# Kernel optimization log

Hardware: AMD Instinct MI355X
Metric: run time of the kernel (lower is better)

Reference implementation:

```python
import jax, jax.numpy as jnp
import numpy as np
import math

B, NB, HID, KD, NH = 256, 16, 512, 64, 8

def setup_inputs() -> dict:
    key = jax.random.key(0)
    ks = jax.random.split(key, 6)
    s = lambda fan_in: 1.0 / math.sqrt(fan_in)
    return {
        "h": jax.random.normal(ks[0], (B, NB, HID), dtype=jnp.float32),
        "mask": jax.random.randint(ks[1], (B, NB), 0, 2, dtype=jnp.int32),
        "Wk": jax.random.normal(ks[2], (NB, HID, KD * NH), dtype=jnp.float32) * s(HID),
        "Wq": jax.random.normal(ks[3], (NB, HID, KD * NH), dtype=jnp.float32) * s(HID),
        "Wv": jax.random.normal(ks[4], (NB, HID, HID * NH), dtype=jnp.float32) * s(HID),
        "Wo": jax.random.normal(ks[5], (NB, HID * NH, HID), dtype=jnp.float32) * s(HID * NH),
    }

def _group_linear(x, w):
    # x: (B, NB, din), w: (NB, din, dout) -> (B, NB, dout)
    return jnp.einsum('bnd,nde->bne', x, w)

def reference(h, mask, Wk, Wq, Wv, Wo):
    # grouped QKV projections
    k = _group_linear(h, Wk).reshape(B, NB, NH, KD).transpose(0, 2, 1, 3)    # (B,H,NB,KD)
    q = _group_linear(h, Wq).reshape(B, NB, NH, KD).transpose(0, 2, 1, 3)    # (B,H,NB,KD)
    v = _group_linear(h, Wv).reshape(B, NB, NH, HID).transpose(0, 2, 1, 3)   # (B,H,NB,HID)
    scores = jnp.einsum('bhqd,bhkd->bhqk', q, k) / math.sqrt(KD)             # (B,H,NB,NB)
    probs = jax.nn.softmax(scores, axis=-1)
    # post-softmax row mask: mask (B,NB) -> (B,1,NB,1)
    probs = probs * mask.astype(probs.dtype)[:, None, :, None]
    ctx = jnp.einsum('bhqk,bhkd->bhqd', probs, v)                            # (B,H,NB,HID)
    ctx = ctx.transpose(0, 2, 1, 3).reshape(B, NB, NH * HID)                 # (B,NB,H*HID)
    return _group_linear(ctx, Wo)                                            # (B,NB,HID)
```

## Files before the change

kernel.cpp:

```cpp
#include <hip/hip_runtime.h>


typedef short s16x4 __attribute__((ext_vector_type(4)));
typedef short s16x8 __attribute__((ext_vector_type(8)));
typedef float f32x4 __attribute__((ext_vector_type(4)));

__device__ __forceinline__ unsigned short f2bf(float f) {
  unsigned int u = __builtin_bit_cast(unsigned int, f);
  u += 0x7fffu + ((u >> 16) & 1u);
  return (unsigned short)(u >> 16);
}
__device__ __forceinline__ float bf2f(unsigned short s) {
  unsigned int u = ((unsigned int)s) << 16;
  return __builtin_bit_cast(float, u);
}

__global__ __launch_bounds__(256) void cvt_h(const float* __restrict__ h,
                                             unsigned short* __restrict__ hb)
{
  int i = (blockIdx.x * 256 + threadIdx.x) * 4;
  float4 v = *reinterpret_cast<const float4*>(h + i);
  s16x4 st = { (short)f2bf(v.x), (short)f2bf(v.y), (short)f2bf(v.z), (short)f2bf(v.w) };
  *reinterpret_cast<s16x4*>(hb + i) = st;
}

__global__ __launch_bounds__(256) void qkv_gemm(
    const unsigned short* __restrict__ hb, const float* __restrict__ Wq,
    const float* __restrict__ Wk, const float* __restrict__ Wv,
    unsigned short* __restrict__ qo, unsigned short* __restrict__ ko,
    unsigned short* __restrict__ vo)
{
  const int g    = blockIdx.y;
  const int n0   = blockIdx.x * 64;
  const int tid  = threadIdx.x;
  const int lane = tid & 63;
  const int wave = tid >> 6;
  const int wm   = wave * 64;

  const float* W; unsigned short* out; size_t obase; int oldc, wN, c0;
  if (n0 < 512)       { W = Wq + (size_t)g * 262144;  out = qo; obase = (size_t)g * 512;  oldc = 8192;  wN = 512;  c0 = n0; }
  else if (n0 < 1024) { W = Wk + (size_t)g * 262144;  out = ko; obase = (size_t)g * 512;  oldc = 8192;  wN = 512;  c0 = n0 - 512; }
  else                { W = Wv + (size_t)g * 2097152; out = vo; obase = (size_t)g * 4096; oldc = 65536; wN = 4096; c0 = n0 - 1024; }

  const unsigned short* A = hb + (size_t)g * 512;

  __shared__ unsigned short As[256][32];
  __shared__ unsigned short Bs[64][36];

  f32x4 acc[4][4];
  #pragma unroll
  for (int i = 0; i < 4; i++)
    #pragma unroll
    for (int j = 0; j < 4; j++) acc[i][j] = (f32x4){0.f, 0.f, 0.f, 0.f};

  const int fr = lane & 15, fq = lane >> 4;

  for (int k0 = 0; k0 < 512; k0 += 32) {
    __syncthreads();
    #pragma unroll
    for (int p = 0; p < 4; p++) {
      int idx = p * 256 + tid;
      int row = idx >> 2, kq = idx & 3;
      *reinterpret_cast<s16x8*>(&As[row][kq * 8]) =
          *reinterpret_cast<const s16x8*>(A + (size_t)row * 8192 + k0 + kq * 8);
    }
    #pragma unroll
    for (int p = 0; p < 2; p++) {
      int idx = p * 256 + tid;
      int n = idx & 63, kc = idx >> 6;
      const float* wp = W + (size_t)(k0 + kc * 4) * wN + c0 + n;
      float w0 = wp[0], w1 = wp[wN], w2 = wp[2 * wN], w3 = wp[3 * wN];
      s16x4 st = { (short)f2bf(w0), (short)f2bf(w1), (short)f2bf(w2), (short)f2bf(w3) };
      *reinterpret_cast<s16x4*>(&Bs[n][kc * 4]) = st;
    }
    __syncthreads();
    s16x8 af[4], bfr[4];
    #pragma unroll
    for (int mi = 0; mi < 4; mi++)
      af[mi] = *reinterpret_cast<const s16x8*>(&As[wm + mi * 16 + fr][fq * 8]);
    #pragma unroll
    for (int ni = 0; ni < 4; ni++) {
      const s16x4* bp = reinterpret_cast<const s16x4*>(&Bs[ni * 16 + fr][fq * 8]);
      s16x4 lo = bp[0], hi = bp[1];
      bfr[ni] = __builtin_shufflevector(lo, hi, 0, 1, 2, 3, 4, 5, 6, 7);
    }
    #pragma unroll
    for (int mi = 0; mi < 4; mi++)
      #pragma unroll
      for (int ni = 0; ni < 4; ni++)
        acc[mi][ni] = __builtin_amdgcn_mfma_f32_16x16x32_bf16(af[mi], bfr[ni], acc[mi][ni], 0, 0, 0);
  }

  #pragma unroll
  for (int mi = 0; mi < 4; mi++)
    #pragma unroll
    for (int ni = 0; ni < 4; ni++)
      #pragma unroll
      for (int r = 0; r < 4; r++) {
        int row = wm + mi * 16 + fq * 4 + r;
        int col = c0 + ni * 16 + fr;
        out[obase + (size_t)row * oldc + col] = f2bf(acc[mi][ni][r]);
      }
}

__global__ __launch_bounds__(256) void attn_kernel(
    const unsigned short* __restrict__ q, const unsigned short* __restrict__ k,
    const unsigned short* __restrict__ v, const int* __restrict__ mask,
    unsigned short* __restrict__ ctx)
{
  const int b  = blockIdx.x >> 3;
  const int hh = blockIdx.x & 7;
  const int tid = threadIdx.x;

  __shared__ float qs[16][65];
  __shared__ float ks[16][65];
  __shared__ float sc[16][16];

  {
    int n = tid >> 4, d4 = (tid & 15) * 4;
    size_t gi = ((size_t)(b * 16 + n) << 9) + (hh << 6) + d4;
    ushort4 qv = *reinterpret_cast<const ushort4*>(q + gi);
    ushort4 kv = *reinterpret_cast<const ushort4*>(k + gi);
    qs[n][d4] = bf2f(qv.x); qs[n][d4+1] = bf2f(qv.y); qs[n][d4+2] = bf2f(qv.z); qs[n][d4+3] = bf2f(qv.w);
    ks[n][d4] = bf2f(kv.x); ks[n][d4+1] = bf2f(kv.y); ks[n][d4+2] = bf2f(kv.z); ks[n][d4+3] = bf2f(kv.w);
  }
  __syncthreads();
  {
    int qi = tid >> 4, ki = tid & 15;
    float s = 0.f;
    #pragma unroll
    for (int j = 0; j < 64; j++) s += qs[qi][j] * ks[ki][j];
    sc[qi][ki] = s * 0.125f;
  }
  __syncthreads();
  if (tid < 16) {
    float m = sc[tid][0];
    #pragma unroll
    for (int j = 1; j < 16; j++) m = fmaxf(m, sc[tid][j]);
    float ev[16], sum = 0.f;
    #pragma unroll
    for (int j = 0; j < 16; j++) { ev[j] = __expf(sc[tid][j] - m); sum += ev[j]; }
    float scale = (mask[b * 16 + tid] != 0) ? (1.f / sum) : 0.f;
    #pragma unroll
    for (int j = 0; j < 16; j++) sc[tid][j] = ev[j] * scale;
  }
  __syncthreads();
  {
    int col4  = (tid & 127) * 4;
    int qbase = (tid >> 7) * 8;
    float a0[8], a1[8], a2[8], a3[8];
    #pragma unroll
    for (int j = 0; j < 8; j++) { a0[j] = 0.f; a1[j] = 0.f; a2[j] = 0.f; a3[j] = 0.f; }
    #pragma unroll
    for (int kk = 0; kk < 16; kk++) {
      ushort4 vv = *reinterpret_cast<const ushort4*>(
          v + ((size_t)(b * 16 + kk) << 12) + (hh << 9) + col4);
      float v0 = bf2f(vv.x), v1 = bf2f(vv.y), v2 = bf2f(vv.z), v3 = bf2f(vv.w);
      #pragma unroll
      for (int j = 0; j < 8; j++) {
        float p = sc[qbase + j][kk];
        a0[j] += p * v0; a1[j] += p * v1; a2[j] += p * v2; a3[j] += p * v3;
      }
    }
    #pragma unroll
    for (int j = 0; j < 8; j++) {
      ushort4 st = { f2bf(a0[j]), f2bf(a1[j]), f2bf(a2[j]), f2bf(a3[j]) };
      *reinterpret_cast<ushort4*>(
          ctx + ((size_t)(b * 16 + qbase + j) << 12) + (hh << 9) + col4) = st;
    }
  }
}

__global__ __launch_bounds__(512) void out_gemm(
    const unsigned short* __restrict__ ctxp, const float* __restrict__ Wo,
    float* __restrict__ partial)
{
  const int g    = blockIdx.y;
  const int bx   = blockIdx.x;
  const int sk   = bx >> 3;
  const int n0   = (bx & 7) * 64;
  const int tid  = threadIdx.x;
  const int lane = tid & 63;
  const int wave = tid >> 6;
  const int wm   = (wave >> 1) * 64;
  const int wn   = (wave & 1) * 32;

  const unsigned short* A = ctxp + (size_t)g * 4096;
  const float* W = Wo + (size_t)g * 2097152;

  __shared__ unsigned short As[256][32];
  __shared__ unsigned short Bs[64][36];

  f32x4 acc[4][2];
  #pragma unroll
  for (int i = 0; i < 4; i++)
    #pragma unroll
    for (int j = 0; j < 2; j++) acc[i][j] = (f32x4){0.f, 0.f, 0.f, 0.f};

  const int fr = lane & 15, fq = lane >> 4;
  const int kend = sk * 1024 + 1024;

  for (int k0 = sk * 1024; k0 < kend; k0 += 32) {
    __syncthreads();
    #pragma unroll
    for (int p = 0; p < 2; p++) {
      int idx = p * 512 + tid;
      int row = idx >> 2, kq = idx & 3;
      *reinterpret_cast<s16x8*>(&As[row][kq * 8]) =
          *reinterpret_cast<const s16x8*>(A + (size_t)row * 65536 + k0 + kq * 8);
    }
    {
      int n = tid & 63, kc = tid >> 6;
      const float* wp = W + (size_t)(k0 + kc * 4) * 512 + n0 + n;
      float w0 = wp[0], w1 = wp[512], w2 = wp[1024], w3 = wp[1536];
      s16x4 st = { (short)f2bf(w0), (short)f2bf(w1), (short)f2bf(w2), (short)f2bf(w3) };
      *reinterpret_cast<s16x4*>(&Bs[n][kc * 4]) = st;
    }
    __syncthreads();
    s16x8 af[4], bfr[2];
    #pragma unroll
    for (int mi = 0; mi < 4; mi++)
      af[mi] = *reinterpret_cast<const s16x8*>(&As[wm + mi * 16 + fr][fq * 8]);
    #pragma unroll
    for (int ni = 0; ni < 2; ni++) {
      const s16x4* bp = reinterpret_cast<const s16x4*>(&Bs[wn + ni * 16 + fr][fq * 8]);
      s16x4 lo = bp[0], hi = bp[1];
      bfr[ni] = __builtin_shufflevector(lo, hi, 0, 1, 2, 3, 4, 5, 6, 7);
    }
    #pragma unroll
    for (int mi = 0; mi < 4; mi++)
      #pragma unroll
      for (int ni = 0; ni < 2; ni++)
        acc[mi][ni] = __builtin_amdgcn_mfma_f32_16x16x32_bf16(af[mi], bfr[ni], acc[mi][ni], 0, 0, 0);
  }

  float* pg = partial + (size_t)sk * 2097152 + (size_t)g * 512;
  #pragma unroll
  for (int mi = 0; mi < 4; mi++)
    #pragma unroll
    for (int ni = 0; ni < 2; ni++)
      #pragma unroll
      for (int r = 0; r < 4; r++) {
        int row = wm + mi * 16 + fq * 4 + r;
        int col = n0 + wn + ni * 16 + fr;
        pg[(size_t)row * 8192 + col] = acc[mi][ni][r];
      }
}

__global__ __launch_bounds__(256) void reduce4(const float* __restrict__ part,
                                               float* __restrict__ out)
{
  int i = (blockIdx.x * 256 + threadIdx.x) * 4;
  float4 a = *reinterpret_cast<const float4*>(part + i);
  float4 b = *reinterpret_cast<const float4*>(part + 2097152 + i);
  float4 c = *reinterpret_cast<const float4*>(part + 4194304 + i);
  float4 d = *reinterpret_cast<const float4*>(part + 6291456 + i);
  float4 s = { a.x + b.x + c.x + d.x, a.y + b.y + c.y + d.y,
               a.z + b.z + c.z + d.z, a.w + b.w + c.w + d.w };
  *reinterpret_cast<float4*>(out + i) = s;
}

extern "C" void kernel_launch(void* const* d_in, const int* in_sizes, int n_in,
                              void* d_out, int out_size, void* d_ws, size_t ws_size,
                              hipStream_t stream) {
  const float* h  = (const float*)d_in[0];
  const int* mask = (const int*)d_in[1];
  const float* Wk = (const float*)d_in[2];
  const float* Wq = (const float*)d_in[3];
  const float* Wv = (const float*)d_in[4];
  const float* Wo = (const float*)d_in[5];
  float* out = (float*)d_out;

  unsigned short* qws   = (unsigned short*)d_ws;
  unsigned short* kws   = qws + 2097152;
  unsigned short* vws   = kws + 2097152;
  unsigned short* ctxws = vws + 16777216;
  unsigned short* hb    = ctxws;
  float* part           = (float*)d_ws;

  cvt_h<<<2048, 256, 0, stream>>>(h, hb);
  qkv_gemm<<<dim3(80, 16), 256, 0, stream>>>(hb, Wq, Wk, Wv, qws, kws, vws);
  attn_kernel<<<2048, 256, 0, stream>>>(qws, kws, vws, mask, ctxws);
  out_gemm<<<dim3(32, 16), 512, 0, stream>>>(ctxws, Wo, part);
  reduce4<<<2048, 256, 0, stream>>>(part, out);
}
```

Before: 388.0 us.

## Retile QKV and output GEMMs to 128x128 with register prefetch and atomic split-K

Both grouped GEMMs now use 128x128 output tiles with 64-deep K steps and 8 waves per block. The next K tile is prefetched into registers with vectorized float4 weight loads while MFMAs run on the current shared-memory tile. The output GEMM splits K eight ways and accumulates into a zeroed output with atomicAdd, which removes the partial-sum buffer and the separate reduce kernel. In exchange it adds atomic contention, a memset and nondeterministic summation order, and the larger tiles may lower occupancy.

```diff
diff --git a/kernel.cpp b/kernel.cpp
--- a/kernel.cpp
+++ b/kernel.cpp
@@ -24,81 +24,105 @@
   *reinterpret_cast<s16x4*>(hb + i) = st;
 }
 
-__global__ __launch_bounds__(256) void qkv_gemm(
+__global__ __launch_bounds__(512) void qkv_gemm(
     const unsigned short* __restrict__ hb, const float* __restrict__ Wq,
     const float* __restrict__ Wk, const float* __restrict__ Wv,
     unsigned short* __restrict__ qo, unsigned short* __restrict__ ko,
     unsigned short* __restrict__ vo)
 {
   const int g    = blockIdx.y;
-  const int n0   = blockIdx.x * 64;
+  const int bx   = blockIdx.x;
+  const int m0   = (bx / 40) * 128;
+  const int n0   = (bx % 40) * 128;
   const int tid  = threadIdx.x;
   const int lane = tid & 63;
   const int wave = tid >> 6;
-  const int wm   = wave * 64;
+  const int wm   = (wave >> 2) * 64;
+  const int wn   = (wave & 3) * 32;
 
   const float* W; unsigned short* out; size_t obase; int oldc, wN, c0;
   if (n0 < 512)       { W = Wq + (size_t)g * 262144;  out = qo; obase = (size_t)g * 512;  oldc = 8192;  wN = 512;  c0 = n0; }
   else if (n0 < 1024) { W = Wk + (size_t)g * 262144;  out = ko; obase = (size_t)g * 512;  oldc = 8192;  wN = 512;  c0 = n0 - 512; }
   else                { W = Wv + (size_t)g * 2097152; out = vo; obase = (size_t)g * 4096; oldc = 65536; wN = 4096; c0 = n0 - 1024; }
 
-  const unsigned short* A = hb + (size_t)g * 512;
-
-  __shared__ unsigned short As[256][32];
-  __shared__ unsigned short Bs[64][36];
-
-  f32x4 acc[4][4];
+  const unsigned short* A = hb + (size_t)g * 512 + (size_t)m0 * 8192;
+
+  __shared__ unsigned short As[128][64];
+  __shared__ unsigned short Bs[128][64];
+
+  f32x4 acc[4][2];
   #pragma unroll
   for (int i = 0; i < 4; i++)
     #pragma unroll
-    for (int j = 0; j < 4; j++) acc[i][j] = (f32x4){0.f, 0.f, 0.f, 0.f};
+    for (int j = 0; j < 2; j++) acc[i][j] = (f32x4){0.f, 0.f, 0.f, 0.f};
 
   const int fr = lane & 15, fq = lane >> 4;
-
-  for (int k0 = 0; k0 < 512; k0 += 32) {
+  const int bn  = (tid & 31) * 4;
+  const int bkr = tid >> 5;
+
+  s16x8 areg[2];
+  f32x4 breg[4];
+
+  #pragma unroll
+  for (int p = 0; p < 2; p++) {
+    int idx = p * 512 + tid, row = idx >> 3, kq = idx & 7;
+    areg[p] = *reinterpret_cast<const s16x8*>(A + (size_t)row * 8192 + kq * 8);
+  }
+  #pragma unroll
+  for (int l = 0; l < 4; l++)
+    breg[l] = *reinterpret_cast<const f32x4*>(W + (size_t)(bkr * 4 + l) * wN + c0 + bn);
+
+  for (int s = 0; s < 8; ++s) {
+    const int k0 = s * 64;
+    if (s) __syncthreads();
+    #pragma unroll
+    for (int p = 0; p < 2; p++) {
+      int idx = p * 512 + tid, row = idx >> 3, kq = idx & 7;
+      *reinterpret_cast<s16x8*>(&As[row][kq * 8]) = areg[p];
+    }
+    #pragma unroll
+    for (int j = 0; j < 4; j++) {
+      s16x4 st = { (short)f2bf(breg[0][j]), (short)f2bf(breg[1][j]),
+                   (short)f2bf(breg[2][j]), (short)f2bf(breg[3][j]) };
+      *reinterpret_cast<s16x4*>(&Bs[bn + j][bkr * 4]) = st;
+    }
     __syncthreads();
-    #pragma unroll
-    for (int p = 0; p < 4; p++) {
-      int idx = p * 256 + tid;
-      int row = idx >> 2, kq = idx & 3;
-      *reinterpret_cast<s16x8*>(&As[row][kq * 8]) =
-          *reinterpret_cast<const s16x8*>(A + (size_t)row * 8192 + k0 + kq * 8);
-    }
-    #pragma unroll
-    for (int p = 0; p < 2; p++) {
-      int idx = p * 256 + tid;
-      int n = idx & 63, kc = idx >> 6;
-      const float* wp = W + (size_t)(k0 + kc * 4) * wN + c0 + n;
-      float w0 = wp[0], w1 = wp[wN], w2 = wp[2 * wN], w3 = wp[3 * wN];
-      s16x4 st = { (short)f2bf(w0), (short)f2bf(w1), (short)f2bf(w2), (short)f2bf(w3) };
-      *reinterpret_cast<s16x4*>(&Bs[n][kc * 4]) = st;
-    }
-    __syncthreads();
-    s16x8 af[4], bfr[4];
-    #pragma unroll
-    for (int mi = 0; mi < 4; mi++)
-      af[mi] = *reinterpret_cast<const s16x8*>(&As[wm + mi * 16 + fr][fq * 8]);
-    #pragma unroll
-    for (int ni = 0; ni < 4; ni++) {
-      const s16x4* bp = reinterpret_cast<const s16x4*>(&Bs[ni * 16 + fr][fq * 8]);
-      s16x4 lo = bp[0], hi = bp[1];
-      bfr[ni] = __builtin_shufflevector(lo, hi, 0, 1, 2, 3, 4, 5, 6, 7);
-    }
-    #pragma unroll
-    for (int mi = 0; mi < 4; mi++)
-      #pragma unroll
-      for (int ni = 0; ni < 4; ni++)
-        acc[mi][ni] = __builtin_amdgcn_mfma_f32_16x16x32_bf16(af[mi], bfr[ni], acc[mi][ni], 0, 0, 0);
+    if (s < 7) {
+      const int kn = k0 + 64;
+      #pragma unroll
+      for (int p = 0; p < 2; p++) {
+        int idx = p * 512 + tid, row = idx >> 3, kq = idx & 7;
+        areg[p] = *reinterpret_cast<const s16x8*>(A + (size_t)row * 8192 + kn + kq * 8);
+      }
+      #pragma unroll
+      for (int l = 0; l < 4; l++)
+        breg[l] = *reinterpret_cast<const f32x4*>(W + (size_t)(kn + bkr * 4 + l) * wN + c0 + bn);
+    }
+    #pragma unroll
+    for (int half = 0; half < 2; half++) {
+      s16x8 af[4], bfr[2];
+      #pragma unroll
+      for (int mi = 0; mi < 4; mi++)
+        af[mi] = *reinterpret_cast<const s16x8*>(&As[wm + mi * 16 + fr][half * 32 + fq * 8]);
+      #pragma unroll
+      for (int ni = 0; ni < 2; ni++)
+        bfr[ni] = *reinterpret_cast<const s16x8*>(&Bs[wn + ni * 16 + fr][half * 32 + fq * 8]);
+      #pragma unroll
+      for (int mi = 0; mi < 4; mi++)
+        #pragma unroll
+        for (int ni = 0; ni < 2; ni++)
+          acc[mi][ni] = __builtin_amdgcn_mfma_f32_16x16x32_bf16(af[mi], bfr[ni], acc[mi][ni], 0, 0, 0);
+    }
   }
 
   #pragma unroll
   for (int mi = 0; mi < 4; mi++)
     #pragma unroll
-    for (int ni = 0; ni < 4; ni++)
+    for (int ni = 0; ni < 2; ni++)
       #pragma unroll
       for (int r = 0; r < 4; r++) {
-        int row = wm + mi * 16 + fq * 4 + r;
-        int col = c0 + ni * 16 + fr;
+        int row = m0 + wm + mi * 16 + fq * 4 + r;
+        int col = c0 + wn + ni * 16 + fr;
         out[obase + (size_t)row * oldc + col] = f2bf(acc[mi][ni][r]);
       }
 }
@@ -173,23 +197,24 @@
 
 __global__ __launch_bounds__(512) void out_gemm(
     const unsigned short* __restrict__ ctxp, const float* __restrict__ Wo,
-    float* __restrict__ partial)
+    float* __restrict__ outp)
 {
   const int g    = blockIdx.y;
   const int bx   = blockIdx.x;
   const int sk   = bx >> 3;
-  const int n0   = (bx & 7) * 64;
+  const int m0   = ((bx >> 2) & 1) * 128;
+  const int n0   = (bx & 3) * 128;
   const int tid  = threadIdx.x;
   const int lane = tid & 63;
   const int wave = tid >> 6;
-  const int wm   = (wave >> 1) * 64;
-  const int wn   = (wave & 1) * 32;
-
-  const unsigned short* A = ctxp + (size_t)g * 4096;
+  const int wm   = (wave >> 2) * 64;
+  const int wn   = (wave & 3) * 32;
+
+  const unsigned short* A = ctxp + (size_t)g * 4096 + (size_t)m0 * 65536;
   const float* W = Wo + (size_t)g * 2097152;
 
-  __shared__ unsigned short As[256][32];
-  __shared__ unsigned short Bs[64][36];
+  __shared__ unsigned short As[128][64];
+  __shared__ unsigned short Bs[128][64];
 
   f32x4 acc[4][2];
   #pragma unroll
@@ -198,66 +223,76 @@
     for (int j = 0; j < 2; j++) acc[i][j] = (f32x4){0.f, 0.f, 0.f, 0.f};
 
   const int fr = lane & 15, fq = lane >> 4;
-  const int kend = sk * 1024 + 1024;
-
-  for (int k0 = sk * 1024; k0 < kend; k0 += 32) {
+  const int bn  = (tid & 31) * 4;
+  const int bkr = tid >> 5;
+  const int kbase = sk * 512;
+
+  s16x8 areg[2];
+  f32x4 breg[4];
+
+  #pragma unroll
+  for (int p = 0; p < 2; p++) {
+    int idx = p * 512 + tid, row = idx >> 3, kq = idx & 7;
+    areg[p] = *reinterpret_cast<const s16x8*>(A + (size_t)row * 65536 + kbase + kq * 8);
+  }
+  #pragma unroll
+  for (int l = 0; l < 4; l++)
+    breg[l] = *reinterpret_cast<const f32x4*>(W + (size_t)(kbase + bkr * 4 + l) * 512 + n0 + bn);
+
+  for (int s = 0; s < 8; ++s) {
+    const int k0 = kbase + s * 64;
+    if (s) __syncthreads();
+    #pragma unroll
+    for (int p = 0; p < 2; p++) {
+      int idx = p * 512 + tid, row = idx >> 3, kq = idx & 7;
+      *reinterpret_cast<s16x8*>(&As[row][kq * 8]) = areg[p];
+    }
+    #pragma unroll
+    for (int j = 0; j < 4; j++) {
+      s16x4 st = { (short)f2bf(breg[0][j]), (short)f2bf(breg[1][j]),
+                   (short)f2bf(breg[2][j]), (short)f2bf(breg[3][j]) };
+      *reinterpret_cast<s16x4*>(&Bs[bn + j][bkr * 4]) = st;
+    }
     __syncthreads();
-    #pragma unroll
-    for (int p = 0; p < 2; p++) {
-      int idx = p * 512 + tid;
-      int row = idx >> 2, kq = idx & 3;
-      *reinterpret_cast<s16x8*>(&As[row][kq * 8]) =
-          *reinterpret_cast<const s16x8*>(A + (size_t)row * 65536 + k0 + kq * 8);
-    }
-    {
-      int n = tid & 63, kc = tid >> 6;
-      const float* wp = W + (size_t)(k0 + kc * 4) * 512 + n0 + n;
-      float w0 = wp[0], w1 = wp[512], w2 = wp[1024], w3 = wp[1536];
-      s16x4 st = { (short)f2bf(w0), (short)f2bf(w1), (short)f2bf(w2), (short)f2bf(w3) };
-      *reinterpret_cast<s16x4*>(&Bs[n][kc * 4]) = st;
-    }
-    __syncthreads();
-    s16x8 af[4], bfr[2];
-    #pragma unroll
-    for (int mi = 0; mi < 4; mi++)
-      af[mi] = *reinterpret_cast<const s16x8*>(&As[wm + mi * 16 + fr][fq * 8]);
-    #pragma unroll
-    for (int ni = 0; ni < 2; ni++) {
-      const s16x4* bp = reinterpret_cast<const s16x4*>(&Bs[wn + ni * 16 + fr][fq * 8]);
-      s16x4 lo = bp[0], hi = bp[1];
-      bfr[ni] = __builtin_shufflevector(lo, hi, 0, 1, 2, 3, 4, 5, 6, 7);
-    }
-    #pragma unroll
-    for (int mi = 0; mi < 4; mi++)
+    if (s < 7) {
+      const int kn = k0 + 64;
+      #pragma unroll
+      for (int p = 0; p < 2; p++) {
+        int idx = p * 512 + tid, row = idx >> 3, kq = idx & 7;
+        areg[p] = *reinterpret_cast<const s16x8*>(A + (size_t)row * 65536 + kn + kq * 8);
+      }
+      #pragma unroll
+      for (int l = 0; l < 4; l++)
+        breg[l] = *reinterpret_cast<const f32x4*>(W + (size_t)(kn + bkr * 4 + l) * 512 + n0 + bn);
+    }
+    #pragma unroll
+    for (int half = 0; half < 2; half++) {
+      s16x8 af[4], bfr[2];
+      #pragma unroll
+      for (int mi = 0; mi < 4; mi++)
+        af[mi] = *reinterpret_cast<const s16x8*>(&As[wm + mi * 16 + fr][half * 32 + fq * 8]);
       #pragma unroll
       for (int ni = 0; ni < 2; ni++)
-        acc[mi][ni] = __builtin_amdgcn_mfma_f32_16x16x32_bf16(af[mi], bfr[ni], acc[mi][ni], 0, 0, 0);
-  }
-
-  float* pg = partial + (size_t)sk * 2097152 + (size_t)g * 512;
+        bfr[ni] = *reinterpret_cast<const s16x8*>(&Bs[wn + ni * 16 + fr][half * 32 + fq * 8]);
+      #pragma unroll
+      for (int mi = 0; mi < 4; mi++)
+        #pragma unroll
+        for (int ni = 0; ni < 2; ni++)
+          acc[mi][ni] = __builtin_amdgcn_mfma_f32_16x16x32_bf16(af[mi], bfr[ni], acc[mi][ni], 0, 0, 0);
+    }
+  }
+
+  float* og = outp + (size_t)g * 512;
   #pragma unroll
   for (int mi = 0; mi < 4; mi++)
     #pragma unroll
     for (int ni = 0; ni < 2; ni++)
       #pragma unroll
       for (int r = 0; r < 4; r++) {
-        int row = wm + mi * 16 + fq * 4 + r;
+        int row = m0 + wm + mi * 16 + fq * 4 + r;
         int col = n0 + wn + ni * 16 + fr;
-        pg[(size_t)row * 8192 + col] = acc[mi][ni][r];
-      }
-}
-
-__global__ __launch_bounds__(256) void reduce4(const float* __restrict__ part,
-                                               float* __restrict__ out)
-{
-  int i = (blockIdx.x * 256 + threadIdx.x) * 4;
-  float4 a = *reinterpret_cast<const float4*>(part + i);
-  float4 b = *reinterpret_cast<const float4*>(part + 2097152 + i);
-  float4 c = *reinterpret_cast<const float4*>(part + 4194304 + i);
-  float4 d = *reinterpret_cast<const float4*>(part + 6291456 + i);
-  float4 s = { a.x + b.x + c.x + d.x, a.y + b.y + c.y + d.y,
-               a.z + b.z + c.z + d.z, a.w + b.w + c.w + d.w };
-  *reinterpret_cast<float4*>(out + i) = s;
+        atomicAdd(&og[(size_t)row * 8192 + col], acc[mi][ni][r]);
+      }
 }
 
 extern "C" void kernel_launch(void* const* d_in, const int* in_sizes, int n_in,
@@ -276,11 +311,10 @@
   unsigned short* vws   = kws + 2097152;
   unsigned short* ctxws = vws + 16777216;
   unsigned short* hb    = ctxws;
-  float* part           = (float*)d_ws;
 
   cvt_h<<<2048, 256, 0, stream>>>(h, hb);
-  qkv_gemm<<<dim3(80, 16), 256, 0, stream>>>(hb, Wq, Wk, Wv, qws, kws, vws);
+  hipMemsetAsync(d_out, 0, (size_t)out_size * sizeof(float), stream);
+  qkv_gemm<<<dim3(80, 16), 512, 0, stream>>>(hb, Wq, Wk, Wv, qws, kws, vws);
   attn_kernel<<<2048, 256, 0, stream>>>(qws, kws, vws, mask, ctxws);
-  out_gemm<<<dim3(32, 16), 512, 0, stream>>>(ctxws, Wo, part);
-  reduce4<<<2048, 256, 0, stream>>>(part, out);
-}
+  out_gemm<<<dim3(64, 16), 512, 0, stream>>>(ctxws, Wo, out);
+}
```

Measured after the change: 420.6 us. 8.4% more time.
